# Kernel optimization log

Hardware: AMD Instinct MI355X
Metric: run time of the kernel (lower is better)

Reference implementation:

```python
import jax, jax.numpy as jnp
import numpy as np

B, T, D = 4, 4096, 1024
H = 16
HD = D // H
EPS = 1e-6

def setup_inputs() -> dict:
    key = jax.random.key(0)
    ks = jax.random.split(key, 6)
    s = 1.0 / np.sqrt(D)
    return {
        "x":  jax.random.normal(ks[0], (B, T, D), dtype=jnp.float32),
        "Wq": jax.random.uniform(ks[1], (D, D), dtype=jnp.float32, minval=-s, maxval=s),
        "Wk": jax.random.uniform(ks[2], (D, D), dtype=jnp.float32, minval=-s, maxval=s),
        "Wv": jax.random.uniform(ks[3], (D, D), dtype=jnp.float32, minval=-s, maxval=s),
        "Wo": jax.random.uniform(ks[4], (D, D), dtype=jnp.float32, minval=-s, maxval=s),
        "bo": jax.random.uniform(ks[5], (D,), dtype=jnp.float32, minval=-s, maxval=s),
    }

def _feature(z):
    # elu(z) + 1 (positive feature map)
    return jax.nn.elu(z) + 1.0

def reference(x, Wq, Wk, Wv, Wo, bo):
    b, t, _ = x.shape
    # project and split heads: [B,H,T,HD]
    Q = _feature((x @ Wq.T).reshape(b, t, H, HD).transpose(0, 2, 1, 3))
    K = _feature((x @ Wk.T).reshape(b, t, H, HD).transpose(0, 2, 1, 3))
    V = (x @ Wv.T).reshape(b, t, H, HD).transpose(0, 2, 1, 3)
    # global KV aggregation: [B,H,HD,HD]
    KV = jnp.einsum('bhtd,bhte->bhde', K, V)
    K_sum = K.sum(axis=2)                                  # [B,H,HD]
    Z = jnp.einsum('bhtd,bhd->bht', Q, K_sum) + EPS        # [B,H,T]
    context = jnp.einsum('bhtd,bhde->bhte', Q, KV)         # [B,H,T,HD]
    out = context / Z[..., None]
    out = out.transpose(0, 2, 1, 3).reshape(b, t, H * HD)
    return out @ Wo.T + bo
```

## Files before the change

### kernel.cpp

```cpp
#include <hip/hip_runtime.h>
#include <hip/hip_bf16.h>
#include <cstdint>
#include <cstddef>

typedef unsigned short u16;

static constexpr int Bn = 4, T = 4096, Dm = 1024, H = 16, HDv = 64;
static constexpr int Mrows = Bn * T;
static constexpr int Nfused = 3 * Dm;
#define EPSV 1e-6f

typedef __attribute__((ext_vector_type(8))) short bf16x8;
typedef __attribute__((ext_vector_type(4))) float f32x4;

#if defined(__has_builtin)
#if __has_builtin(__builtin_amdgcn_global_load_lds)
#define HAS_GLL 1
#endif
#endif
#ifndef HAS_GLL
#define HAS_GLL 0
#endif

__device__ inline float b2f(u16 u) {
  union { unsigned i; float f; } v; v.i = ((unsigned)u) << 16; return v.f;
}
__device__ inline u16 f2b(float f) {
  union { float f; unsigned i; } v; v.f = f;
  unsigned r = (v.i + 0x7fffu + ((v.i >> 16) & 1u)) >> 16;
  return (u16)r;
}

__global__ void cast_kernel(const float* __restrict__ in, u16* __restrict__ out, int n4) {
  int i = blockIdx.x * 256 + threadIdx.x;
  if (i >= n4) return;
  float4 v = ((const float4*)in)[i];
  u16 o[4];
  o[0] = f2b(v.x); o[1] = f2b(v.y); o[2] = f2b(v.z); o[3] = f2b(v.w);
  ((uint2*)out)[i] = *(uint2*)o;
}

template<int MODE>
__global__ __launch_bounds__(256) void gemm_bt(
    const u16* __restrict__ A, const u16* __restrict__ Bm,
    u16* __restrict__ Cb, float* __restrict__ Cf,
    const float* __restrict__ bias, int Mdim, int N, int K)
{
  __shared__ __align__(16) u16 As[128 * 64];
  __shared__ __align__(16) u16 Bs[128 * 64];
  const int tid  = threadIdx.x;
  const int lane = tid & 63;
  const int wave = tid >> 6;
  const int wr = (wave >> 1) * 64, wc = (wave & 1) * 64;
  const int m0 = blockIdx.x * 128, n0 = blockIdx.y * 128;
  const bool feat = (MODE == 3) && (n0 < 2 * Dm);

  f32x4 acc[4][4] = {};

  for (int k0 = 0; k0 < K; k0 += 64) {
#pragma unroll
    for (int j = 0; j < 4; ++j) {
      int idx = j * 256 + tid;
      int row = idx >> 3;
      int col = (idx & 7) << 3;
      const u16* gA = A  + (size_t)(m0 + row) * K + k0 + col;
      const u16* gB = Bm + (size_t)(n0 + row) * K + k0 + col;
#if HAS_GLL
      __builtin_amdgcn_global_load_lds((const __attribute__((address_space(1))) void*)gA,
                                       (__attribute__((address_space(3))) void*)(As + idx * 8), 16, 0, 0);
      __builtin_amdgcn_global_load_lds((const __attribute__((address_space(1))) void*)gB,
                                       (__attribute__((address_space(3))) void*)(Bs + idx * 8), 16, 0, 0);
#else
      *(uint4*)(As + idx * 8) = *(const uint4*)gA;
      *(uint4*)(Bs + idx * 8) = *(const uint4*)gB;
#endif
    }
    __syncthreads();
#pragma unroll
    for (int kk = 0; kk < 64; kk += 32) {
      bf16x8 af[4], bfv[4];
#pragma unroll
      for (int i = 0; i < 4; ++i) {
        af[i]  = *(const bf16x8*)&As[(wr + i * 16 + (lane & 15)) * 64 + kk + (lane >> 4) * 8];
        bfv[i] = *(const bf16x8*)&Bs[(wc + i * 16 + (lane & 15)) * 64 + kk + (lane >> 4) * 8];
      }
#pragma unroll
      for (int i = 0; i < 4; ++i)
#pragma unroll
        for (int j = 0; j < 4; ++j)
          acc[i][j] = __builtin_amdgcn_mfma_f32_16x16x32_bf16(af[i], bfv[j], acc[i][j], 0, 0, 0);
    }
    __syncthreads();
  }

#pragma unroll
  for (int i = 0; i < 4; ++i) {
#pragma unroll
    for (int j = 0; j < 4; ++j) {
#pragma unroll
      for (int r = 0; r < 4; ++r) {
        int row = m0 + wr + i * 16 + (lane >> 4) * 4 + r;
        int col = n0 + wc + j * 16 + (lane & 15);
        float v = acc[i][j][r];
        if (MODE == 2) {
          Cf[(size_t)row * N + col] = v + bias[col];
        } else {
          if (feat) v = (v > 0.f) ? (v + 1.f) : __expf(v);
          Cb[(size_t)row * N + col] = f2b(v);
        }
      }
    }
  }
}

__global__ __launch_bounds__(256) void kv_kernel(
    const u16* __restrict__ Kb, const u16* __restrict__ Vb, int ldr,
    float* __restrict__ KV, float* __restrict__ Ksum)
{
  const int bh = blockIdx.x;
  const int b = bh >> 4, h = bh & 15;
  const int chunk = blockIdx.y;
  __shared__ __align__(16) float Ks[32][64];
  __shared__ __align__(16) float Vs[32][64];
  const int tid = threadIdx.x;
  const int dq = tid >> 4, eq = tid & 15;
  float acc[4][4] = {};
  float ksum[4] = {};
  const int srow = tid >> 3, scol = (tid & 7) << 3;

  for (int tile = 0; tile < 16; ++tile) {
    const int t0 = chunk * 512 + tile * 32;
    const u16* gK = Kb + ((size_t)(b * T + t0 + srow)) * ldr + h * HDv + scol;
    const u16* gV = Vb + ((size_t)(b * T + t0 + srow)) * ldr + h * HDv + scol;
    uint4 ku = *(const uint4*)gK;
    uint4 vu = *(const uint4*)gV;
    __syncthreads();
    u16* kp = (u16*)&ku; u16* vp = (u16*)&vu;
#pragma unroll
    for (int q = 0; q < 8; ++q) { Ks[srow][scol + q] = b2f(kp[q]); Vs[srow][scol + q] = b2f(vp[q]); }
    __syncthreads();
#pragma unroll
    for (int tt = 0; tt < 32; ++tt) {
      f32x4 kv = *(const f32x4*)&Ks[tt][dq * 4];
      f32x4 vv = *(const f32x4*)&Vs[tt][eq * 4];
#pragma unroll
      for (int i = 0; i < 4; ++i)
#pragma unroll
        for (int j = 0; j < 4; ++j)
          acc[i][j] += kv[i] * vv[j];
    }
#pragma unroll
    for (int s = 0; s < 2; ++s) {
      f32x4 kv = *(const f32x4*)&Ks[eq * 2 + s][dq * 4];
#pragma unroll
      for (int i = 0; i < 4; ++i) ksum[i] += kv[i];
    }
  }
  float* KVp = KV + (size_t)bh * HDv * HDv;
#pragma unroll
  for (int i = 0; i < 4; ++i)
#pragma unroll
    for (int j = 0; j < 4; ++j)
      atomicAdd(&KVp[(dq * 4 + i) * HDv + eq * 4 + j], acc[i][j]);
#pragma unroll
  for (int i = 0; i < 4; ++i) atomicAdd(&Ksum[bh * HDv + dq * 4 + i], ksum[i]);
}

__global__ __launch_bounds__(256) void ctx_kernel(
    const u16* __restrict__ Qb, int ldr, const float* __restrict__ KV,
    const float* __restrict__ Ksum, u16* __restrict__ ctx)
{
  const int bh = blockIdx.x;
  const int b = bh >> 4, h = bh & 15;
  const int t0 = blockIdx.y * 64;
  __shared__ __align__(16) float KVs[64][64];
  __shared__ __align__(16) float Qs[64][68];
  __shared__ float Ksm[64];
  const int tid = threadIdx.x;
  const float* KVg = KV + (size_t)bh * 4096;
#pragma unroll
  for (int j = 0; j < 4; ++j) {
    int idx = j * 256 + tid;
    ((f32x4*)KVs)[idx] = ((const f32x4*)KVg)[idx];
  }
  if (tid < 64) Ksm[tid] = Ksum[bh * HDv + tid];
#pragma unroll
  for (int j = 0; j < 2; ++j) {
    int c = j * 256 + tid;
    int row = c >> 3, col = (c & 7) << 3;
    uint4 qu = *(const uint4*)(Qb + ((size_t)(b * T + t0 + row)) * ldr + h * HDv + col);
    u16* qp = (u16*)&qu;
#pragma unroll
    for (int q = 0; q < 8; ++q) Qs[row][col + q] = b2f(qp[q]);
  }
  __syncthreads();
  const int tq = tid >> 2, e0 = (tid & 3) * 16;
  f32x4 acc[4] = {};
  float z = 0.f;
#pragma unroll
  for (int d = 0; d < 64; ++d) {
    float q = Qs[tq][d];
    z += q * Ksm[d];
#pragma unroll
    for (int j = 0; j < 4; ++j) {
      f32x4 kv = *(const f32x4*)&KVs[d][e0 + j * 4];
      acc[j] += q * kv;
    }
  }
  float inv = 1.f / (z + EPSV);
  u16 o[16];
#pragma unroll
  for (int j = 0; j < 4; ++j)
#pragma unroll
    for (int r = 0; r < 4; ++r) o[j * 4 + r] = f2b(acc[j][r] * inv);
  u16* dst = ctx + ((size_t)(b * T + t0 + tq)) * Dm + h * HDv + e0;
  *(uint4*)dst = *(uint4*)&o[0];
  *(uint4*)(dst + 8) = *(uint4*)&o[8];
}

extern "C" void kernel_launch(void* const* d_in, const int* in_sizes, int n_in,
                              void* d_out, int out_size, void* d_ws, size_t ws_size,
                              hipStream_t stream)
{
  const float* x  = (const float*)d_in[0];
  const float* Wq = (const float*)d_in[1];
  const float* Wk = (const float*)d_in[2];
  const float* Wv = (const float*)d_in[3];
  const float* Wo = (const float*)d_in[4];
  const float* bo = (const float*)d_in[5];
  float* out = (float*)d_out;

  char* ws = (char*)d_ws;
  size_t off = 0;
  auto alloc = [&](size_t bytes) -> void* {
    void* p = ws + off;
    off += (bytes + 255) & ~(size_t)255;
    return p;
  };
  u16* xb   = (u16*)alloc((size_t)Mrows * Dm * 2);
  u16* Wcat = (u16*)alloc((size_t)Nfused * Dm * 2);
  u16* Wob  = (u16*)alloc((size_t)Dm * Dm * 2);
  u16* QKV  = (u16*)alloc((size_t)Mrows * Nfused * 2);
  float* KV   = (float*)alloc((size_t)Bn * H * HDv * HDv * 4);
  float* Ksum = (float*)alloc((size_t)Bn * H * HDv * 4);
  u16* ctx = xb;

  {
    int n4 = Mrows * Dm / 4;
    cast_kernel<<<(n4 + 255) / 256, 256, 0, stream>>>(x, xb, n4);
    int w4 = Dm * Dm / 4;
    cast_kernel<<<(w4 + 255) / 256, 256, 0, stream>>>(Wq, Wcat, w4);
    cast_kernel<<<(w4 + 255) / 256, 256, 0, stream>>>(Wk, Wcat + (size_t)Dm * Dm, w4);
    cast_kernel<<<(w4 + 255) / 256, 256, 0, stream>>>(Wv, Wcat + (size_t)2 * Dm * Dm, w4);
    cast_kernel<<<(w4 + 255) / 256, 256, 0, stream>>>(Wo, Wob, w4);
  }

  gemm_bt<3><<<dim3(Mrows / 128, Nfused / 128), 256, 0, stream>>>(
      xb, Wcat, QKV, nullptr, nullptr, Mrows, Nfused, Dm);

  hipMemsetAsync(KV, 0, ((size_t)Bn * H * HDv * HDv + (size_t)Bn * H * HDv) * 4, stream);

  kv_kernel<<<dim3(Bn * H, 8), 256, 0, stream>>>(QKV + Dm, QKV + 2 * Dm, Nfused, KV, Ksum);
  ctx_kernel<<<dim3(Bn * H, T / 64), 256, 0, stream>>>(QKV, Nfused, KV, Ksum, ctx);

  gemm_bt<2><<<dim3(Mrows / 128, Dm / 128), 256, 0, stream>>>(
      ctx, Wob, nullptr, out, bo, Mrows, Dm, Dm);
}
```

Baseline: 499.5 us.

## Pipeline GEMM with triple-buffered LDS ring, XOR swizzle and 256x128 tiles

Rewrites the bf16 GEMM main loop to use a three-stage LDS ring filled by global_load_lds, with explicit vmcnt waits, so loads for tile t+2 overlap MFMA work on tile t. The LDS layout is XOR-swizzled to reduce bank conflicts on fragment reads, and the block grows to 512 threads covering a 256x128 output tile, with s_setprio around the MFMA bursts. The goal is to hide global memory latency and cut the per-iteration double barrier. In exchange the block uses 144KB of LDS, which limits occupancy to one block per CU, and the code now depends on the global_load_lds builtin with no fallback.

```diff
diff --git a/kernel.cpp b/kernel.cpp
--- a/kernel.cpp
+++ b/kernel.cpp
@@ -12,15 +12,6 @@
 
 typedef __attribute__((ext_vector_type(8))) short bf16x8;
 typedef __attribute__((ext_vector_type(4))) float f32x4;
-
-#if defined(__has_builtin)
-#if __has_builtin(__builtin_amdgcn_global_load_lds)
-#define HAS_GLL 1
-#endif
-#endif
-#ifndef HAS_GLL
-#define HAS_GLL 0
-#endif
 
 __device__ inline float b2f(u16 u) {
   union { unsigned i; float f; } v; v.i = ((unsigned)u) << 16; return v.f;
@@ -40,57 +31,96 @@
   ((uint2*)out)[i] = *(uint2*)o;
 }
 
+#define RING_TILE 49152
+#define RING_BYTES (3 * RING_TILE)
+
 template<int MODE>
-__global__ __launch_bounds__(256) void gemm_bt(
+__global__ __launch_bounds__(512) void gemm_bt(
     const u16* __restrict__ A, const u16* __restrict__ Bm,
     u16* __restrict__ Cb, float* __restrict__ Cf,
     const float* __restrict__ bias, int Mdim, int N, int K)
 {
-  __shared__ __align__(16) u16 As[128 * 64];
-  __shared__ __align__(16) u16 Bs[128 * 64];
+  __shared__ __align__(16) u16 lds[RING_BYTES / 2];
   const int tid  = threadIdx.x;
   const int lane = tid & 63;
-  const int wave = tid >> 6;
-  const int wr = (wave >> 1) * 64, wc = (wave & 1) * 64;
-  const int m0 = blockIdx.x * 128, n0 = blockIdx.y * 128;
+  const int wid  = tid >> 6;
+  const int wr = (wid & 3) * 64;
+  const int wc = (wid >> 2) * 64;
+  const int m0 = blockIdx.x * 256, n0 = blockIdx.y * 128;
   const bool feat = (MODE == 3) && (n0 < 2 * Dm);
 
   f32x4 acc[4][4] = {};
-
-  for (int k0 = 0; k0 < K; k0 += 64) {
-#pragma unroll
-    for (int j = 0; j < 4; ++j) {
-      int idx = j * 256 + tid;
-      int row = idx >> 3;
-      int col = (idx & 7) << 3;
-      const u16* gA = A  + (size_t)(m0 + row) * K + k0 + col;
-      const u16* gB = Bm + (size_t)(n0 + row) * K + k0 + col;
-#if HAS_GLL
-      __builtin_amdgcn_global_load_lds((const __attribute__((address_space(1))) void*)gA,
-                                       (__attribute__((address_space(3))) void*)(As + idx * 8), 16, 0, 0);
-      __builtin_amdgcn_global_load_lds((const __attribute__((address_space(1))) void*)gB,
-                                       (__attribute__((address_space(3))) void*)(Bs + idx * 8), 16, 0, 0);
-#else
-      *(uint4*)(As + idx * 8) = *(const uint4*)gA;
-      *(uint4*)(Bs + idx * 8) = *(const uint4*)gB;
-#endif
-    }
-    __syncthreads();
-#pragma unroll
-    for (int kk = 0; kk < 64; kk += 32) {
-      bf16x8 af[4], bfv[4];
+  const int nt = K >> 6;
+
+  auto stage = [&](int t, int rb) {
+    const int k0 = t << 6;
+#pragma unroll
+    for (int l = 0; l < 4; ++l) {
+      int c = l * 512 + tid;
+      int r = c >> 3;
+      int sl = (c & 7) ^ (r & 7);
+      const u16* g = A + (size_t)(m0 + r) * K + k0 + sl * 8;
+      __builtin_amdgcn_global_load_lds(
+          (const __attribute__((address_space(1))) void*)g,
+          (__attribute__((address_space(3))) void*)((char*)lds + rb + c * 16),
+          16, 0, 0);
+    }
+#pragma unroll
+    for (int l = 0; l < 2; ++l) {
+      int c = l * 512 + tid;
+      int r = c >> 3;
+      int sl = (c & 7) ^ (r & 7);
+      const u16* g = Bm + (size_t)(n0 + r) * K + k0 + sl * 8;
+      __builtin_amdgcn_global_load_lds(
+          (const __attribute__((address_space(1))) void*)g,
+          (__attribute__((address_space(3))) void*)((char*)lds + rb + 32768 + c * 16),
+          16, 0, 0);
+    }
+  };
+
+  stage(0, 0);
+  if (nt > 1) stage(1, RING_TILE);
+
+  int rb = 0;
+  for (int t = 0; t < nt; ++t) {
+    if (t + 1 < nt) {
+      asm volatile("s_waitcnt vmcnt(6)" ::: "memory");
+    } else {
+      asm volatile("s_waitcnt vmcnt(0)" ::: "memory");
+    }
+    __builtin_amdgcn_s_barrier();
+    asm volatile("" ::: "memory");
+
+    if (t + 2 < nt) {
+      int rb2 = rb + 2 * RING_TILE;
+      if (rb2 >= RING_BYTES) rb2 -= RING_BYTES;
+      stage(t + 2, rb2);
+    }
+
+    const char* Abase = (const char*)lds + rb;
+    const char* Bbase = (const char*)lds + rb + 32768;
+#pragma unroll
+    for (int ks = 0; ks < 2; ++ks) {
+      bf16x8 af[4], bf[4];
+      const int cb = ks * 64 + (lane >> 4) * 16;
 #pragma unroll
       for (int i = 0; i < 4; ++i) {
-        af[i]  = *(const bf16x8*)&As[(wr + i * 16 + (lane & 15)) * 64 + kk + (lane >> 4) * 8];
-        bfv[i] = *(const bf16x8*)&Bs[(wc + i * 16 + (lane & 15)) * 64 + kk + (lane >> 4) * 8];
+        int ar = wr + i * 16 + (lane & 15);
+        af[i] = *(const bf16x8*)(Abase + ar * 128 + (cb ^ ((ar & 7) << 4)));
+        int br = wc + i * 16 + (lane & 15);
+        bf[i] = *(const bf16x8*)(Bbase + br * 128 + (cb ^ ((br & 7) << 4)));
       }
+      __builtin_amdgcn_s_setprio(1);
 #pragma unroll
       for (int i = 0; i < 4; ++i)
 #pragma unroll
         for (int j = 0; j < 4; ++j)
-          acc[i][j] = __builtin_amdgcn_mfma_f32_16x16x32_bf16(af[i], bfv[j], acc[i][j], 0, 0, 0);
-    }
-    __syncthreads();
+          acc[i][j] = __builtin_amdgcn_mfma_f32_16x16x32_bf16(af[i], bf[j], acc[i][j], 0, 0, 0);
+      __builtin_amdgcn_s_setprio(0);
+    }
+
+    rb += RING_TILE;
+    if (rb == RING_BYTES) rb = 0;
   }
 
 #pragma unroll
@@ -255,7 +285,7 @@
     cast_kernel<<<(w4 + 255) / 256, 256, 0, stream>>>(Wo, Wob, w4);
   }
 
-  gemm_bt<3><<<dim3(Mrows / 128, Nfused / 128), 256, 0, stream>>>(
+  gemm_bt<3><<<dim3(Mrows / 256, Nfused / 128), 512, 0, stream>>>(
       xb, Wcat, QKV, nullptr, nullptr, Mrows, Nfused, Dm);
 
   hipMemsetAsync(KV, 0, ((size_t)Bn * H * HDv * HDv + (size_t)Bn * H * HDv) * 4, stream);
@@ -263,6 +293,6 @@
   kv_kernel<<<dim3(Bn * H, 8), 256, 0, stream>>>(QKV + Dm, QKV + 2 * Dm, Nfused, KV, Ksum);
   ctx_kernel<<<dim3(Bn * H, T / 64), 256, 0, stream>>>(QKV, Nfused, KV, Ksum, ctx);
 
-  gemm_bt<2><<<dim3(Mrows / 128, Dm / 128), 256, 0, stream>>>(
+  gemm_bt<2><<<dim3(Mrows / 256, Dm / 128), 512, 0, stream>>>(
       ctx, Wob, nullptr, out, bo, Mrows, Dm, Dm);
 }
```

After: 444.6 us. 1.12x faster.
